# Performance work log

Measured on AMD Instinct MI355X. Metric: run time of the kernel, lower is better.

The kernel has to match this reference:

```python
import jax, jax.numpy as jnp
import numpy as np

NUM_ITERATIONS = 5
DEPTH_L = 2
NUM_NODES = 8448
MAX_CHECK_NEIGHBORS = 10
BATCH = 1024


def setup_inputs() -> dict:
    key = jax.random.key(0)
    k1, k2, k3 = jax.random.split(key, 3)
    input_llr = jax.random.normal(k1, (BATCH, NUM_NODES), dtype=jnp.float32)
    w_ch = jnp.ones((NUM_NODES,), dtype=jnp.float32)
    w_res = jnp.ones((DEPTH_L, NUM_NODES), dtype=jnp.float32)
    check_index_tensor = jax.random.randint(k2, (NUM_NODES, MAX_CHECK_NEIGHBORS), 0, NUM_NODES, dtype=jnp.int32)
    var_index_tensor = jax.random.randint(k3, (NUM_NODES, MAX_CHECK_NEIGHBORS), 0, NUM_NODES, dtype=jnp.int32)
    return {"input_llr": input_llr, "w_ch": w_ch, "w_res": w_res,
            "check_index_tensor": check_index_tensor, "var_index_tensor": var_index_tensor}


def _check_layer(var_messages, check_index_tensor):
    # Gather neighbor variable messages: (B, N, K)
    gathered = var_messages[:, check_index_tensor]
    # tanh-product BP check-node update, numerically clipped
    t = jnp.tanh(jnp.clip(0.5 * gathered, -9.9, 9.9))
    prod = jnp.prod(t, axis=-1)  # (B, N)
    prod = jnp.clip(prod, -0.999999, 0.999999)
    return 2.0 * jnp.arctanh(prod)


def reference(input_llr, w_ch, w_res, check_index_tensor, var_index_tensor):
    weighted_llr = input_llr * w_ch[None, :]
    var_messages = weighted_llr
    prev = []  # deque(maxlen=DEPTH_L), newest first
    for _ in range(NUM_ITERATIONS):
        prev.insert(0, var_messages)
        prev = prev[:DEPTH_L]
        check_messages = _check_layer(var_messages, check_index_tensor)
        residual = sum(w_res[l][None, :] * prev[l] for l in range(len(prev)))
        var_messages = weighted_llr + check_messages + residual
    soft_bits = jax.nn.sigmoid(var_messages + input_llr)
    return soft_bits
```

## Files before the change

kernel.cpp:

```cpp
#include <hip/hip_runtime.h>


#define NN    8448
#define MAXNB 10
#define TPB   1024
#define MAXK  9
#define ITERS 5
#define LDS_BYTES  (NN * 2 * (int)sizeof(float))
#define OFFS_INTS  12
#define OFFS_BYTES ((size_t)NN * OFFS_INTS * sizeof(int))
#define W4_BYTES   ((size_t)NN * 4 * sizeof(float))
#define WS_NEEDED  (OFFS_BYTES + W4_BYTES)

typedef float v2f __attribute__((ext_vector_type(2)));

__global__ __launch_bounds__(256)
void prep_kernel(const int* __restrict__ cidx, const float* __restrict__ w_ch,
                 const float* __restrict__ w_res, int* __restrict__ offs,
                 float4* __restrict__ w4)
{
    int n = blockIdx.x * 256 + threadIdx.x;
    if (n < NN) {
        #pragma unroll
        for (int j = 0; j < MAXNB; ++j)
            offs[n * OFFS_INTS + j] = cidx[n * MAXNB + j] * 8;
        offs[n * OFFS_INTS + 10] = 0;
        offs[n * OFFS_INTS + 11] = 0;
        w4[n] = make_float4(w_ch[n], w_res[n], w_res[NN + n], 0.0f);
    }
}

template<bool USE_OFF>
__global__ __launch_bounds__(TPB)
void ldpc_decode_kernel(const float* __restrict__ input_llr,
                        const float* __restrict__ w_ch,
                        const float* __restrict__ w_res,
                        const int*   __restrict__ cidx,
                        const int*   __restrict__ offs,
                        const float4* __restrict__ w4,
                        float* __restrict__ out)
{
    extern __shared__ char smem[];
    v2f* __restrict__ t2 = (v2f*)smem;
    const char* __restrict__ smbase = smem;
    const int tid  = threadIdx.x;
    const int row0 = blockIdx.x * 2;
    const float* __restrict__ in0 = input_llr + (size_t)row0 * NN;
    const float* __restrict__ in1 = in0 + NN;
    float* __restrict__ out0 = out + (size_t)row0 * NN;
    float* __restrict__ out1 = out0 + NN;

    float vm0[MAXK], vm1[MAXK], vmp0[MAXK], vmp1[MAXK];

    #pragma unroll
    for (int k = 0; k < MAXK; ++k) {
        int n = tid + k * TPB;
        vmp0[k] = 0.0f; vmp1[k] = 0.0f;
        vm0[k] = 0.0f;  vm1[k] = 0.0f;
        if (k < MAXK - 1 || n < NN) {
            float wc = w_ch[n];
            vm0[k] = in0[n] * wc;
            vm1[k] = in1[n] * wc;
        }
    }

    for (int it = 0; it < ITERS; ++it) {
        #pragma unroll
        for (int k = 0; k < MAXK; ++k) {
            int n = tid + k * TPB;
            if (k < MAXK - 1 || n < NN) {
                float y0 = fminf(fmaxf(vm0[k], -19.8f), 19.8f);
                float y1 = fminf(fmaxf(vm1[k], -19.8f), 19.8f);
                float A = __expf(y0) + 1.0f;
                float B = __expf(y1) + 1.0f;
                float r = __builtin_amdgcn_rcpf(A * B);
                v2f t;
                t.x = fmaf(r * B, -2.0f, 1.0f);
                t.y = fmaf(r * A, -2.0f, 1.0f);
                t2[n] = t;
            }
        }
        __syncthreads();

        #pragma unroll 1
        for (int k = 0; k < MAXK; ++k) {
            int n = tid + k * TPB;
            if (n < NN) {
                int oa0, oa1, oa2, oa3, oa4, ob0, ob1, ob2, ob3, ob4;
                if (USE_OFF) {
                    const int4* op = (const int4*)(offs + n * OFFS_INTS);
                    int4 oA = op[0];
                    int4 oB = op[1];
                    int2 oC = ((const int2*)op)[4];
                    oa0 = oA.x; ob0 = oA.y; oa1 = oA.z; ob1 = oA.w;
                    oa2 = oB.x; ob2 = oB.y; oa3 = oB.z; ob3 = oB.w;
                    oa4 = oC.x; ob4 = oC.y;
                } else {
                    const int2* ip = (const int2*)(cidx + n * MAXNB);
                    int2 i0 = ip[0], i1 = ip[1], i2 = ip[2], i3 = ip[3], i4 = ip[4];
                    oa0 = i0.x << 3; ob0 = i0.y << 3;
                    oa1 = i1.x << 3; ob1 = i1.y << 3;
                    oa2 = i2.x << 3; ob2 = i2.y << 3;
                    oa3 = i3.x << 3; ob3 = i3.y << 3;
                    oa4 = i4.x << 3; ob4 = i4.y << 3;
                }
                v2f a0 = *(const v2f*)(smbase + oa0);
                v2f b0 = *(const v2f*)(smbase + ob0);
                v2f a1 = *(const v2f*)(smbase + oa1);
                v2f b1 = *(const v2f*)(smbase + ob1);
                v2f a2 = *(const v2f*)(smbase + oa2);
                v2f b2 = *(const v2f*)(smbase + ob2);
                v2f a3 = *(const v2f*)(smbase + oa3);
                v2f b3 = *(const v2f*)(smbase + ob3);
                v2f a4 = *(const v2f*)(smbase + oa4);
                v2f b4 = *(const v2f*)(smbase + ob4);
                v2f m01 = (a0 * b0) * (a1 * b1);
                v2f m23 = (a2 * b2) * (a3 * b3);
                v2f pr  = (m01 * m23) * (a4 * b4);
                pr = __builtin_elementwise_min(
                         __builtin_elementwise_max(pr, (v2f)(-0.999999f)),
                         (v2f)(0.999999f));
                v2f num = 1.0f + pr;
                v2f den = 1.0f - pr;
                float check0 = 0.69314718f * (__log2f(num.x) - __log2f(den.x));
                float check1 = 0.69314718f * (__log2f(num.y) - __log2f(den.y));
                float wc, wr0, wr1;
                if (USE_OFF) {
                    float4 w = w4[n];
                    wc = w.x; wr0 = w.y; wr1 = w.z;
                } else {
                    wc = w_ch[n]; wr0 = w_res[n]; wr1 = w_res[NN + n];
                }
                float x0 = in0[n];
                float x1 = in1[n];
                float nv0 = fmaf(x0, wc, check0) + fmaf(wr0, vm0[k], wr1 * vmp0[k]);
                float nv1 = fmaf(x1, wc, check1) + fmaf(wr0, vm1[k], wr1 * vmp1[k]);
                vmp0[k] = vm0[k]; vm0[k] = nv0;
                vmp1[k] = vm1[k]; vm1[k] = nv1;
            }
        }
        __syncthreads();
    }

    #pragma unroll
    for (int k = 0; k < MAXK; ++k) {
        int n = tid + k * TPB;
        if (k < MAXK - 1 || n < NN) {
            float x0 = vm0[k] + in0[n];
            float x1 = vm1[k] + in1[n];
            out0[n] = __fdividef(1.0f, 1.0f + __expf(-x0));
            out1[n] = __fdividef(1.0f, 1.0f + __expf(-x1));
        }
    }
}

extern "C" void kernel_launch(void* const* d_in, const int* in_sizes, int n_in,
                              void* d_out, int out_size, void* d_ws, size_t ws_size,
                              hipStream_t stream) {
    const float* input_llr = (const float*)d_in[0];
    const float* w_ch      = (const float*)d_in[1];
    const float* w_res     = (const float*)d_in[2];
    const int*   cidx      = (const int*)d_in[3];
    float* out = (float*)d_out;
    int batch = in_sizes[0] / NN;
    const bool use_off = (ws_size >= WS_NEEDED) && (d_ws != nullptr);

    hipFuncSetAttribute((const void*)ldpc_decode_kernel<true>,
                        hipFuncAttributeMaxDynamicSharedMemorySize, LDS_BYTES);
    hipFuncSetAttribute((const void*)ldpc_decode_kernel<false>,
                        hipFuncAttributeMaxDynamicSharedMemorySize, LDS_BYTES);

    if (use_off) {
        int*    offs = (int*)d_ws;
        float4* w4   = (float4*)((char*)d_ws + OFFS_BYTES);
        hipLaunchKernelGGL(prep_kernel, dim3((NN + 255) / 256), dim3(256), 0,
                           stream, cidx, w_ch, w_res, offs, w4);
        hipLaunchKernelGGL(ldpc_decode_kernel<true>, dim3(batch / 2), dim3(TPB),
                           LDS_BYTES, stream, input_llr, w_ch, w_res, cidx,
                           offs, w4, out);
    } else {
        hipLaunchKernelGGL(ldpc_decode_kernel<false>, dim3(batch / 2), dim3(TPB),
                           LDS_BYTES, stream, input_llr, w_ch, w_res, cidx,
                           nullptr, nullptr, out);
    }
}
```

Before: 160.3 us.

## Double-buffer tanh table in LDS and fuse tanh into the check-update pass

Uses two LDS tables so each iteration reads the previous tanh table and writes the next one in the same loop, which removes one barrier per iteration and the separate tanh pass. The weighted channel LLR is kept in registers instead of reloading the input from global memory each iteration. The residual weights are packed into the padding slots of the offset table, dropping the w4 buffer. The cost is double the LDS per block (about 135 KB), which may limit occupancy, plus extra registers for the cached weighted LLR.

Measured after the change: 151.0 us. 5.8% less time.

```diff
diff --git a/kernel.cpp b/kernel.cpp
--- a/kernel.cpp
+++ b/kernel.cpp
@@ -6,28 +6,40 @@
 #define TPB   1024
 #define MAXK  9
 #define ITERS 5
-#define LDS_BYTES  (NN * 2 * (int)sizeof(float))
+#define TBL_BYTES  (NN * 8)
+#define LDS_BYTES  (2 * TBL_BYTES)
 #define OFFS_INTS  12
 #define OFFS_BYTES ((size_t)NN * OFFS_INTS * sizeof(int))
-#define W4_BYTES   ((size_t)NN * 4 * sizeof(float))
-#define WS_NEEDED  (OFFS_BYTES + W4_BYTES)
+#define WS_NEEDED  OFFS_BYTES
 
 typedef float v2f __attribute__((ext_vector_type(2)));
 
 __global__ __launch_bounds__(256)
-void prep_kernel(const int* __restrict__ cidx, const float* __restrict__ w_ch,
-                 const float* __restrict__ w_res, int* __restrict__ offs,
-                 float4* __restrict__ w4)
+void prep_kernel(const int* __restrict__ cidx, const float* __restrict__ w_res,
+                 int* __restrict__ offs)
 {
     int n = blockIdx.x * 256 + threadIdx.x;
     if (n < NN) {
         #pragma unroll
         for (int j = 0; j < MAXNB; ++j)
             offs[n * OFFS_INTS + j] = cidx[n * MAXNB + j] * 8;
-        offs[n * OFFS_INTS + 10] = 0;
-        offs[n * OFFS_INTS + 11] = 0;
-        w4[n] = make_float4(w_ch[n], w_res[n], w_res[NN + n], 0.0f);
+        offs[n * OFFS_INTS + 10] = __float_as_int(w_res[n]);
+        offs[n * OFFS_INTS + 11] = __float_as_int(w_res[NN + n]);
     }
+}
+
+__device__ __forceinline__ v2f tanh_half(v2f v)
+{
+    v2f y = __builtin_elementwise_min(
+                __builtin_elementwise_max(v, (v2f)(-19.8f)), (v2f)(19.8f));
+    v2f e;
+    e.x = __expf(y.x);
+    e.y = __expf(y.y);
+    v2f ab = e + 1.0f;
+    float r = __builtin_amdgcn_rcpf(ab.x * ab.y);
+    v2f ba = ab.yx;
+    v2f inv = ba * r;
+    return 1.0f - 2.0f * inv;
 }
 
 template<bool USE_OFF>
@@ -37,12 +49,9 @@
                         const float* __restrict__ w_res,
                         const int*   __restrict__ cidx,
                         const int*   __restrict__ offs,
-                        const float4* __restrict__ w4,
                         float* __restrict__ out)
 {
     extern __shared__ char smem[];
-    v2f* __restrict__ t2 = (v2f*)smem;
-    const char* __restrict__ smbase = smem;
     const int tid  = threadIdx.x;
     const int row0 = blockIdx.x * 2;
     const float* __restrict__ in0 = input_llr + (size_t)row0 * NN;
@@ -50,104 +59,104 @@
     float* __restrict__ out0 = out + (size_t)row0 * NN;
     float* __restrict__ out1 = out0 + NN;
 
-    float vm0[MAXK], vm1[MAXK], vmp0[MAXK], vmp1[MAXK];
+    v2f wllr[MAXK], vm[MAXK], vmp[MAXK];
 
     #pragma unroll
     for (int k = 0; k < MAXK; ++k) {
         int n = tid + k * TPB;
-        vmp0[k] = 0.0f; vmp1[k] = 0.0f;
-        vm0[k] = 0.0f;  vm1[k] = 0.0f;
+        wllr[k] = (v2f)(0.0f);
+        vmp[k]  = (v2f)(0.0f);
         if (k < MAXK - 1 || n < NN) {
             float wc = w_ch[n];
-            vm0[k] = in0[n] * wc;
-            vm1[k] = in1[n] * wc;
+            v2f x;
+            x.x = in0[n];
+            x.y = in1[n];
+            wllr[k] = x * wc;
+        }
+        vm[k] = wllr[k];
+        if (k < MAXK - 1 || n < NN) {
+            v2f t = tanh_half(vm[k]);
+            *(v2f*)(smem + (size_t)n * 8) = t;
         }
     }
+    __syncthreads();
 
+    #pragma unroll
     for (int it = 0; it < ITERS; ++it) {
+        const int rbase = (it & 1) ? TBL_BYTES : 0;
+        const int wbase = (it & 1) ? 0 : TBL_BYTES;
         #pragma unroll
         for (int k = 0; k < MAXK; ++k) {
             int n = tid + k * TPB;
             if (k < MAXK - 1 || n < NN) {
-                float y0 = fminf(fmaxf(vm0[k], -19.8f), 19.8f);
-                float y1 = fminf(fmaxf(vm1[k], -19.8f), 19.8f);
-                float A = __expf(y0) + 1.0f;
-                float B = __expf(y1) + 1.0f;
-                float r = __builtin_amdgcn_rcpf(A * B);
-                v2f t;
-                t.x = fmaf(r * B, -2.0f, 1.0f);
-                t.y = fmaf(r * A, -2.0f, 1.0f);
-                t2[n] = t;
-            }
-        }
-        __syncthreads();
-
-        #pragma unroll 1
-        for (int k = 0; k < MAXK; ++k) {
-            int n = tid + k * TPB;
-            if (n < NN) {
-                int oa0, oa1, oa2, oa3, oa4, ob0, ob1, ob2, ob3, ob4;
+                int o0, o1, o2, o3, o4, o5, o6, o7, o8, o9;
+                float wr0, wr1;
                 if (USE_OFF) {
                     const int4* op = (const int4*)(offs + n * OFFS_INTS);
                     int4 oA = op[0];
                     int4 oB = op[1];
-                    int2 oC = ((const int2*)op)[4];
-                    oa0 = oA.x; ob0 = oA.y; oa1 = oA.z; ob1 = oA.w;
-                    oa2 = oB.x; ob2 = oB.y; oa3 = oB.z; ob3 = oB.w;
-                    oa4 = oC.x; ob4 = oC.y;
+                    int4 oC = op[2];
+                    o0 = oA.x; o1 = oA.y; o2 = oA.z; o3 = oA.w;
+                    o4 = oB.x; o5 = oB.y; o6 = oB.z; o7 = oB.w;
+                    o8 = oC.x; o9 = oC.y;
+                    wr0 = __int_as_float(oC.z);
+                    wr1 = __int_as_float(oC.w);
                 } else {
                     const int2* ip = (const int2*)(cidx + n * MAXNB);
                     int2 i0 = ip[0], i1 = ip[1], i2 = ip[2], i3 = ip[3], i4 = ip[4];
-                    oa0 = i0.x << 3; ob0 = i0.y << 3;
-                    oa1 = i1.x << 3; ob1 = i1.y << 3;
-                    oa2 = i2.x << 3; ob2 = i2.y << 3;
-                    oa3 = i3.x << 3; ob3 = i3.y << 3;
-                    oa4 = i4.x << 3; ob4 = i4.y << 3;
+                    o0 = i0.x << 3; o1 = i0.y << 3;
+                    o2 = i1.x << 3; o3 = i1.y << 3;
+                    o4 = i2.x << 3; o5 = i2.y << 3;
+                    o6 = i3.x << 3; o7 = i3.y << 3;
+                    o8 = i4.x << 3; o9 = i4.y << 3;
+                    wr0 = w_res[n];
+                    wr1 = w_res[NN + n];
                 }
-                v2f a0 = *(const v2f*)(smbase + oa0);
-                v2f b0 = *(const v2f*)(smbase + ob0);
-                v2f a1 = *(const v2f*)(smbase + oa1);
-                v2f b1 = *(const v2f*)(smbase + ob1);
-                v2f a2 = *(const v2f*)(smbase + oa2);
-                v2f b2 = *(const v2f*)(smbase + ob2);
-                v2f a3 = *(const v2f*)(smbase + oa3);
-                v2f b3 = *(const v2f*)(smbase + ob3);
-                v2f a4 = *(const v2f*)(smbase + oa4);
-                v2f b4 = *(const v2f*)(smbase + ob4);
-                v2f m01 = (a0 * b0) * (a1 * b1);
-                v2f m23 = (a2 * b2) * (a3 * b3);
-                v2f pr  = (m01 * m23) * (a4 * b4);
+                const char* __restrict__ rb = smem + rbase;
+                v2f g0 = *(const v2f*)(rb + o0);
+                v2f g1 = *(const v2f*)(rb + o1);
+                v2f g2 = *(const v2f*)(rb + o2);
+                v2f g3 = *(const v2f*)(rb + o3);
+                v2f g4 = *(const v2f*)(rb + o4);
+                v2f g5 = *(const v2f*)(rb + o5);
+                v2f g6 = *(const v2f*)(rb + o6);
+                v2f g7 = *(const v2f*)(rb + o7);
+                v2f g8 = *(const v2f*)(rb + o8);
+                v2f g9 = *(const v2f*)(rb + o9);
+                v2f m01 = (g0 * g1) * (g2 * g3);
+                v2f m23 = (g4 * g5) * (g6 * g7);
+                v2f pr  = (m01 * m23) * (g8 * g9);
                 pr = __builtin_elementwise_min(
                          __builtin_elementwise_max(pr, (v2f)(-0.999999f)),
                          (v2f)(0.999999f));
                 v2f num = 1.0f + pr;
                 v2f den = 1.0f - pr;
-                float check0 = 0.69314718f * (__log2f(num.x) - __log2f(den.x));
-                float check1 = 0.69314718f * (__log2f(num.y) - __log2f(den.y));
-                float wc, wr0, wr1;
-                if (USE_OFF) {
-                    float4 w = w4[n];
-                    wc = w.x; wr0 = w.y; wr1 = w.z;
-                } else {
-                    wc = w_ch[n]; wr0 = w_res[n]; wr1 = w_res[NN + n];
+                v2f ln, ld;
+                ln.x = __log2f(num.x);
+                ln.y = __log2f(num.y);
+                ld.x = __log2f(den.x);
+                ld.y = __log2f(den.y);
+                v2f check = (ln - ld) * 0.69314718f;
+                v2f res = vm[k] * wr0 + vmp[k] * wr1;
+                v2f nv  = (wllr[k] + check) + res;
+                vmp[k] = vm[k];
+                vm[k]  = nv;
+                if (it < ITERS - 1) {
+                    v2f t = tanh_half(nv);
+                    *(v2f*)(smem + wbase + (size_t)n * 8) = t;
                 }
-                float x0 = in0[n];
-                float x1 = in1[n];
-                float nv0 = fmaf(x0, wc, check0) + fmaf(wr0, vm0[k], wr1 * vmp0[k]);
-                float nv1 = fmaf(x1, wc, check1) + fmaf(wr0, vm1[k], wr1 * vmp1[k]);
-                vmp0[k] = vm0[k]; vm0[k] = nv0;
-                vmp1[k] = vm1[k]; vm1[k] = nv1;
             }
+            __builtin_amdgcn_sched_barrier(0);
         }
-        __syncthreads();
+        if (it < ITERS - 1) __syncthreads();
     }
 
     #pragma unroll
     for (int k = 0; k < MAXK; ++k) {
         int n = tid + k * TPB;
         if (k < MAXK - 1 || n < NN) {
-            float x0 = vm0[k] + in0[n];
-            float x1 = vm1[k] + in1[n];
+            float x0 = vm[k].x + in0[n];
+            float x1 = vm[k].y + in1[n];
             out0[n] = __fdividef(1.0f, 1.0f + __expf(-x0));
             out1[n] = __fdividef(1.0f, 1.0f + __expf(-x1));
         }
@@ -171,16 +180,15 @@
                         hipFuncAttributeMaxDynamicSharedMemorySize, LDS_BYTES);
 
     if (use_off) {
-        int*    offs = (int*)d_ws;
-        float4* w4   = (float4*)((char*)d_ws + OFFS_BYTES);
+        int* offs = (int*)d_ws;
         hipLaunchKernelGGL(prep_kernel, dim3((NN + 255) / 256), dim3(256), 0,
-                           stream, cidx, w_ch, w_res, offs, w4);
+                           stream, cidx, w_res, offs);
         hipLaunchKernelGGL(ldpc_decode_kernel<true>, dim3(batch / 2), dim3(TPB),
                            LDS_BYTES, stream, input_llr, w_ch, w_res, cidx,
-                           offs, w4, out);
+                           offs, out);
     } else {
         hipLaunchKernelGGL(ldpc_decode_kernel<false>, dim3(batch / 2), dim3(TPB),
                            LDS_BYTES, stream, input_llr, w_ch, w_res, cidx,
-                           nullptr, nullptr, out);
+                           nullptr, out);
     }
 }
```
